# Performance work log

Hardware: AMD Instinct MI355X
Metric: run time of the kernel (lower is better)

Reference implementation:

```python
import jax, jax.numpy as jnp
import numpy as np

C = 64

def _dwconv3d(x, w, b, tdil):
    # x: (B,C,T,H,W); w: (C,1,3,3,3) depthwise; temporal dilation tdil, padding (tdil,1,1)
    y = jax.lax.conv_general_dilated(
        x, w,
        window_strides=(1, 1, 1),
        padding=((tdil, tdil), (1, 1), (1, 1)),
        rhs_dilation=(tdil, 1, 1),
        dimension_numbers=('NCDHW', 'OIDHW', 'NCDHW'),
        feature_group_count=x.shape[1],
    )
    return y + b[None, :, None, None, None]

def _lag_diff(x, k):
    # first k frames kept, rest = x[t] - x[t-k]  (vectorized, no Python loop over T)
    return jnp.concatenate([x[:, :, :k], x[:, :, k:] - x[:, :, :-k]], axis=2)

def setup_inputs() -> dict:
    key = jax.random.key(0)
    ks = jax.random.split(key, 8)
    B, T, H, W = 4, 32, 56, 56
    s = 0.05
    inp = {
        'input': jax.random.normal(ks[0], (B, C, T, H, W), dtype=jnp.float32),
        'w1': jax.random.normal(ks[1], (C, 1, 3, 3, 3), dtype=jnp.float32) * s,
        'b1': jax.random.normal(ks[2], (C,), dtype=jnp.float32) * s,
        'w2': jax.random.normal(ks[3], (C, 1, 3, 3, 3), dtype=jnp.float32) * s,
        'b2': jax.random.normal(ks[4], (C,), dtype=jnp.float32) * s,
        'w3': jax.random.normal(ks[5], (C, 1, 3, 3, 3), dtype=jnp.float32) * s,
        'b3': jax.random.normal(ks[6], (C,), dtype=jnp.float32) * s,
        'weights': jnp.ones((3,), dtype=jnp.float32) / 3.0,
    }
    return inp

def reference(input, w1, b1, w2, b2, w3, b3, weights):
    d1 = _lag_diff(_dwconv3d(input, w1, b1, 1), 1)
    d2 = _lag_diff(_dwconv3d(input, w2, b2, 2), 2)
    d3 = _lag_diff(_dwconv3d(input, w3, b3, 3), 3)
    half = jnp.float32(0.5)
    gate = ((jax.nn.sigmoid(d1) - half) * weights[0]
            + (jax.nn.sigmoid(d2) - half) * weights[1]
            + (jax.nn.sigmoid(d3) - half) * weights[2])
    return input * gate
```

## Files before the change

### kernel.cpp

```cpp
#include <hip/hip_runtime.h>

namespace {

constexpr int T = 32, H = 56, W = 56;
constexpr int HW = H * W;
constexpr int THW = T * HW;
constexpr int GROUPS = H * (W / 2);

template <int N> struct ic { static constexpr int value = N; };

__device__ __forceinline__ float sigm(float x) {
    float e = __expf(-x);
    return __builtin_amdgcn_rcpf(1.0f + e);
}

__global__ __launch_bounds__(64, 3)
void tts_fused(const float* __restrict__ x,
               const float* __restrict__ w1, const float* __restrict__ b1,
               const float* __restrict__ w2, const float* __restrict__ b2,
               const float* __restrict__ w3, const float* __restrict__ b3,
               const float* __restrict__ wm,
               float* __restrict__ out) {
    const int g = blockIdx.x * 64 + threadIdx.x;
    if (g >= GROUPS) return;
    const int bc = blockIdx.y;
    const int h  = g / 28;
    const int wq = g - h * 28;
    const int w0 = wq << 1;

    const float* __restrict__ xbc = x + (size_t)bc * THW;
    float* __restrict__ obc       = out + (size_t)bc * THW;
    const int c = bc & 63;
    const float* __restrict__ wa = w1 + c * 27;
    const float* __restrict__ wb = w2 + c * 27;
    const float* __restrict__ wc = w3 + c * 27;
    const float bias1 = b1[c], bias2 = b2[c], bias3 = b3[c];
    const float W0 = wm[0], W1 = wm[1], W2 = wm[2];
    const float goff = 0.5f * (W0 + W1 + W2);

    const bool vtop = (h >= 1), vbot = (h <= H - 2);
    const bool vl = (wq > 0), vr = (wq < 27);
    const int boff = h * W + w0;

    float cc[7][3][4];
    float p1[2], p2a[2], p2b[2], p3a[2], p3b[2], p3c[2];
#pragma unroll
    for (int p = 0; p < 2; ++p) {
        p1[p] = 0.f; p2a[p] = 0.f; p2b[p] = 0.f;
        p3a[p] = 0.f; p3b[p] = 0.f; p3c[p] = 0.f;
    }

    auto zero_plane = [&](auto Sc) {
        constexpr int s = decltype(Sc)::value;
#pragma unroll
        for (int r = 0; r < 3; ++r)
#pragma unroll
            for (int j = 0; j < 4; ++j) cc[s][r][j] = 0.f;
    };

    auto load_plane = [&](auto Sc, int tp) {
        constexpr int s = decltype(Sc)::value;
        const float* pp = xbc + tp * HW + boff;
#pragma unroll
        for (int r = 0; r < 3; ++r) {
            const bool vrow = (r == 0) ? vtop : ((r == 2) ? vbot : true);
            const float* rp = pp + (r - 1) * W;
            if (vrow) {
                const float2 m = *(const float2*)rp;
                cc[s][r][1] = m.x; cc[s][r][2] = m.y;
                cc[s][r][0] = vl ? rp[-1] : 0.f;
                cc[s][r][3] = vr ? rp[2]  : 0.f;
            } else {
#pragma unroll
                for (int j = 0; j < 4; ++j) cc[s][r][j] = 0.f;
            }
        }
    };

    auto conv9 = [&](float (&acc)[2], auto Sc, const float* __restrict__ wp) {
        constexpr int s = decltype(Sc)::value;
#pragma unroll
        for (int r = 0; r < 3; ++r)
#pragma unroll
            for (int kw = 0; kw < 3; ++kw) {
                const float wg = wp[r * 3 + kw];
#pragma unroll
                for (int p = 0; p < 2; ++p)
                    acc[p] = fmaf(cc[s][r][p + kw], wg, acc[p]);
            }
    };

    zero_plane(ic<4>{}); zero_plane(ic<5>{}); zero_plane(ic<6>{});
    load_plane(ic<0>{}, 0); load_plane(ic<1>{}, 1); load_plane(ic<2>{}, 2);

    auto step = [&](int t, auto Uc) {
        constexpr int u = decltype(Uc)::value;
        constexpr int snew = (u + 3) % 7;
        if (t + 3 < T) load_plane(ic<snew>{}, t + 3);
        else           zero_plane(ic<snew>{});

        float a1[2], a2[2], a3[2];
#pragma unroll
        for (int p = 0; p < 2; ++p) { a1[p] = bias1; a2[p] = bias2; a3[p] = bias3; }

        conv9(a1, ic<(u + 6) % 7>{}, wa);
        conv9(a1, ic<u>{},           wa + 9);
        conv9(a1, ic<(u + 1) % 7>{}, wa + 18);
        conv9(a2, ic<(u + 5) % 7>{}, wb);
        conv9(a2, ic<u>{},           wb + 9);
        conv9(a2, ic<(u + 2) % 7>{}, wb + 18);
        conv9(a3, ic<(u + 4) % 7>{}, wc);
        conv9(a3, ic<u>{},           wc + 9);
        conv9(a3, ic<(u + 3) % 7>{}, wc + 18);

        float2 ov;
        float* ovp = (float*)&ov;
#pragma unroll
        for (int p = 0; p < 2; ++p) {
            const float y1 = a1[p], y2 = a2[p], y3 = a3[p];
            const float d1 = (t >= 1) ? y1 - p1[p]  : y1;
            const float d2 = (t >= 2) ? y2 - p2b[p] : y2;
            const float d3 = (t >= 3) ? y3 - p3c[p] : y3;
            p1[p]  = y1;
            p2b[p] = p2a[p]; p2a[p] = y2;
            p3c[p] = p3b[p]; p3b[p] = p3a[p]; p3a[p] = y3;
            const float gte = fmaf(sigm(d1), W0,
                             fmaf(sigm(d2), W1,
                             fmaf(sigm(d3), W2, -goff)));
            ovp[p] = cc[u][1][p + 1] * gte;
        }
        *(float2*)(obc + t * HW + boff) = ov;
    };

#pragma unroll 1
    for (int tb = 0; tb <= T - 7; tb += 7) {
        step(tb + 0, ic<0>{}); step(tb + 1, ic<1>{}); step(tb + 2, ic<2>{});
        step(tb + 3, ic<3>{}); step(tb + 4, ic<4>{}); step(tb + 5, ic<5>{});
        step(tb + 6, ic<6>{});
    }
    step(28, ic<0>{}); step(29, ic<1>{}); step(30, ic<2>{}); step(31, ic<3>{});
}

}

extern "C" void kernel_launch(void* const* d_in, const int* in_sizes, int n_in,
                              void* d_out, int out_size, void* d_ws, size_t ws_size,
                              hipStream_t stream) {
    (void)in_sizes; (void)n_in; (void)d_ws; (void)ws_size; (void)out_size;
    const float* x  = (const float*)d_in[0];
    const float* w1 = (const float*)d_in[1];
    const float* b1 = (const float*)d_in[2];
    const float* w2 = (const float*)d_in[3];
    const float* b2 = (const float*)d_in[4];
    const float* w3 = (const float*)d_in[5];
    const float* b3 = (const float*)d_in[6];
    const float* wm = (const float*)d_in[7];
    float* out = (float*)d_out;

    tts_fused<<<dim3((GROUPS + 63) / 64, 256), dim3(64), 0, stream>>>(
        x, w1, b1, w2, b2, w3, b3, wm, out);
}
```

Baseline: 272.7 us.

## Use buffer loads with OOB zeroing and packed FP32 FMAs in fused conv kernel

```diff
diff --git a/kernel.cpp b/kernel.cpp
--- a/kernel.cpp
+++ b/kernel.cpp
@@ -5,16 +5,37 @@
 constexpr int T = 32, H = 56, W = 56;
 constexpr int HW = H * W;
 constexpr int THW = T * HW;
+constexpr int PLANE_B = HW * 4;
+constexpr int ROW_B = W * 4;
 constexpr int GROUPS = H * (W / 2);
 
 template <int N> struct ic { static constexpr int value = N; };
+
+typedef float v2f __attribute__((ext_vector_type(2)));
+typedef int   v4i __attribute__((ext_vector_type(4)));
+
+__device__ float buf_load_f32(v4i srd, int voff, int soff, int aux)
+    __asm("llvm.amdgcn.raw.buffer.load.f32");
+__device__ v2f buf_load_v2f(v4i srd, int voff, int soff, int aux)
+    __asm("llvm.amdgcn.raw.buffer.load.v2f32");
+__device__ void buf_store_v2f(v2f v, v4i srd, int voff, int soff, int aux)
+    __asm("llvm.amdgcn.raw.buffer.store.v2f32");
+
+__device__ __forceinline__ v4i make_srd(const void* p, int nrec) {
+    v4i r;
+    r.x = (int)(unsigned long long)p;
+    r.y = (int)((unsigned long long)p >> 32);
+    r.z = nrec;
+    r.w = 0x00020000;
+    return r;
+}
 
 __device__ __forceinline__ float sigm(float x) {
     float e = __expf(-x);
     return __builtin_amdgcn_rcpf(1.0f + e);
 }
 
-__global__ __launch_bounds__(64, 3)
+__global__ __launch_bounds__(64, 2)
 void tts_fused(const float* __restrict__ x,
                const float* __restrict__ w1, const float* __restrict__ b1,
                const float* __restrict__ w2, const float* __restrict__ b2,
@@ -38,56 +59,51 @@
     const float W0 = wm[0], W1 = wm[1], W2 = wm[2];
     const float goff = 0.5f * (W0 + W1 + W2);
 
-    const bool vtop = (h >= 1), vbot = (h <= H - 2);
-    const bool vl = (wq > 0), vr = (wq < 27);
-    const int boff = h * W + w0;
+    const int voffC = (h - 1) * ROW_B + w0 * 4;
+    const int voffL = (wq > 0)  ? voffC - 4 : (1 << 30);
+    const int voffR = (wq < 27) ? voffC + 8 : (1 << 30);
+    const int boff4 = (h * W + w0) * 4;
+    const v4i osrd = make_srd(obc, THW * 4);
 
-    float cc[7][3][4];
-    float p1[2], p2a[2], p2b[2], p3a[2], p3b[2], p3c[2];
-#pragma unroll
-    for (int p = 0; p < 2; ++p) {
-        p1[p] = 0.f; p2a[p] = 0.f; p2b[p] = 0.f;
-        p3a[p] = 0.f; p3b[p] = 0.f; p3c[p] = 0.f;
-    }
+    v2f cc[7][3][2];
+    v2f p1v, p2a, p2b, p3a, p3b, p3c;
+    p1v = 0.f; p2a = 0.f; p2b = 0.f; p3a = 0.f; p3b = 0.f; p3c = 0.f;
 
     auto zero_plane = [&](auto Sc) {
         constexpr int s = decltype(Sc)::value;
 #pragma unroll
-        for (int r = 0; r < 3; ++r)
-#pragma unroll
-            for (int j = 0; j < 4; ++j) cc[s][r][j] = 0.f;
+        for (int r = 0; r < 3; ++r) {
+            cc[s][r][0] = 0.f; cc[s][r][1] = 0.f;
+        }
     };
 
     auto load_plane = [&](auto Sc, int tp) {
         constexpr int s = decltype(Sc)::value;
-        const float* pp = xbc + tp * HW + boff;
+        const v4i srd = make_srd(xbc + tp * HW, PLANE_B);
 #pragma unroll
         for (int r = 0; r < 3; ++r) {
-            const bool vrow = (r == 0) ? vtop : ((r == 2) ? vbot : true);
-            const float* rp = pp + (r - 1) * W;
-            if (vrow) {
-                const float2 m = *(const float2*)rp;
-                cc[s][r][1] = m.x; cc[s][r][2] = m.y;
-                cc[s][r][0] = vl ? rp[-1] : 0.f;
-                cc[s][r][3] = vr ? rp[2]  : 0.f;
-            } else {
-#pragma unroll
-                for (int j = 0; j < 4; ++j) cc[s][r][j] = 0.f;
-            }
+            const float c0 = buf_load_f32(srd, voffL + r * ROW_B, 0, 0);
+            const v2f   m  = buf_load_v2f(srd, voffC + r * ROW_B, 0, 0);
+            const float c3 = buf_load_f32(srd, voffR + r * ROW_B, 0, 0);
+            v2f q0; q0.x = c0;  q0.y = m.x;
+            v2f q1; q1.x = m.y; q1.y = c3;
+            cc[s][r][0] = q0; cc[s][r][1] = q1;
         }
     };
 
-    auto conv9 = [&](float (&acc)[2], auto Sc, const float* __restrict__ wp) {
+    auto conv9 = [&](v2f& acc, auto Sc, const float* __restrict__ wp) {
         constexpr int s = decltype(Sc)::value;
 #pragma unroll
-        for (int r = 0; r < 3; ++r)
-#pragma unroll
-            for (int kw = 0; kw < 3; ++kw) {
-                const float wg = wp[r * 3 + kw];
-#pragma unroll
-                for (int p = 0; p < 2; ++p)
-                    acc[p] = fmaf(cc[s][r][p + kw], wg, acc[p]);
-            }
+        for (int r = 0; r < 3; ++r) {
+            const float wk0 = wp[r * 3 + 0];
+            const float wk1 = wp[r * 3 + 1];
+            const float wk2 = wp[r * 3 + 2];
+            const v2f s0 = {wk0, wk0}, s2 = {wk2, wk2};
+            acc = __builtin_elementwise_fma(cc[s][r][0], s0, acc);
+            acc.x = fmaf(cc[s][r][0].y, wk1, acc.x);
+            acc.y = fmaf(cc[s][r][1].x, wk1, acc.y);
+            acc = __builtin_elementwise_fma(cc[s][r][1], s2, acc);
+        }
     };
 
     zero_plane(ic<4>{}); zero_plane(ic<5>{}); zero_plane(ic<6>{});
@@ -99,9 +115,7 @@
         if (t + 3 < T) load_plane(ic<snew>{}, t + 3);
         else           zero_plane(ic<snew>{});
 
-        float a1[2], a2[2], a3[2];
-#pragma unroll
-        for (int p = 0; p < 2; ++p) { a1[p] = bias1; a2[p] = bias2; a3[p] = bias3; }
+        v2f a1 = {bias1, bias1}, a2 = {bias2, bias2}, a3 = {bias3, bias3};
 
         conv9(a1, ic<(u + 6) % 7>{}, wa);
         conv9(a1, ic<u>{},           wa + 9);
@@ -113,23 +127,21 @@
         conv9(a3, ic<u>{},           wc + 9);
         conv9(a3, ic<(u + 3) % 7>{}, wc + 18);
 
-        float2 ov;
-        float* ovp = (float*)&ov;
-#pragma unroll
-        for (int p = 0; p < 2; ++p) {
-            const float y1 = a1[p], y2 = a2[p], y3 = a3[p];
-            const float d1 = (t >= 1) ? y1 - p1[p]  : y1;
-            const float d2 = (t >= 2) ? y2 - p2b[p] : y2;
-            const float d3 = (t >= 3) ? y3 - p3c[p] : y3;
-            p1[p]  = y1;
-            p2b[p] = p2a[p]; p2a[p] = y2;
-            p3c[p] = p3b[p]; p3b[p] = p3a[p]; p3a[p] = y3;
-            const float gte = fmaf(sigm(d1), W0,
-                             fmaf(sigm(d2), W1,
-                             fmaf(sigm(d3), W2, -goff)));
-            ovp[p] = cc[u][1][p + 1] * gte;
-        }
-        *(float2*)(obc + t * HW + boff) = ov;
+        const v2f d1 = (t >= 1) ? a1 - p1v : a1;
+        const v2f d2 = (t >= 2) ? a2 - p2b : a2;
+        const v2f d3 = (t >= 3) ? a3 - p3c : a3;
+        p1v = a1;
+        p2b = p2a; p2a = a2;
+        p3c = p3b; p3b = p3a; p3a = a3;
+
+        v2f ov;
+        ov.x = cc[u][1][0].y * fmaf(sigm(d1.x), W0,
+                               fmaf(sigm(d2.x), W1,
+                               fmaf(sigm(d3.x), W2, -goff)));
+        ov.y = cc[u][1][1].x * fmaf(sigm(d1.y), W0,
+                               fmaf(sigm(d2.y), W1,
+                               fmaf(sigm(d3.y), W2, -goff)));
+        buf_store_v2f(ov, osrd, boff4, t * PLANE_B, 0);
     };
 
 #pragma unroll 1
```

Result: slower. 293.3 us (+7.6%).
